# Kernel tuning notes

Hardware: AMD Instinct MI355X
Metric: run time of the kernel (lower is better)

The kernel has to match this reference:

```python
import math
import jax, jax.numpy as jnp
import numpy as np

B, T, T_P, C, H = 4, 2048, 256, 768, 12
HD = C // H


def setup_inputs() -> dict:
    key = jax.random.key(0)
    k1, k2, k3, k4 = jax.random.split(key, 4)
    x = jax.random.normal(k1, (B, T, C), dtype=jnp.float32)
    prefix = jax.random.normal(k2, (B, T_P, C), dtype=jnp.float32)
    # torch nn.Linear weight layout: (out_features, in_features)
    W_qkv = jax.random.normal(k3, (3 * C, C), dtype=jnp.float32) * (1.0 / math.sqrt(C))
    W_out = jax.random.normal(k4, (C, C), dtype=jnp.float32) * (1.0 / math.sqrt(C))
    return {"x": x, "prefix": prefix, "W_qkv": W_qkv, "W_out": W_out}


def _mac_causal_mask(t_p: int, t: int) -> jnp.ndarray:
    total = t_p + t
    mask = jnp.zeros((total, total), dtype=bool)
    mask = mask.at[:t_p, t_p:].set(True)  # h tokens blocked from x tokens
    causal = jnp.triu(jnp.ones((t, t), dtype=bool), k=1)  # causal within x block
    return mask.at[t_p:, t_p:].set(causal)


def reference(x, prefix, W_qkv, W_out):
    b, t, c = x.shape
    t_p = prefix.shape[1]
    t_all = t_p + t
    x_full = jnp.concatenate([prefix, x], axis=1)          # (B, T_all, C)
    qkv = x_full @ W_qkv.T                                  # (B, T_all, 3C)
    q, k, v = jnp.split(qkv, 3, axis=-1)
    # (B, H, T_all, HD)
    q = q.reshape(b, t_all, H, HD).transpose(0, 2, 1, 3)
    k = k.reshape(b, t_all, H, HD).transpose(0, 2, 1, 3)
    v = v.reshape(b, t_all, H, HD).transpose(0, 2, 1, 3)
    scale = 1.0 / math.sqrt(HD)
    att = jnp.einsum('bhqd,bhkd->bhqk', q, k) * scale       # (B, H, T_all, T_all)
    mask = _mac_causal_mask(t_p, t)
    att = jnp.where(mask[None, None], -jnp.inf, att)
    att = jax.nn.softmax(att, axis=-1)                      # dropout = identity (eval)
    out = jnp.einsum('bhqk,bhkd->bhqd', att, v)             # (B, H, T_all, HD)
    out = out.transpose(0, 2, 1, 3).reshape(b, t_all, c)
    out = out @ W_out.T
    return out[:, t_p:, :]                                  # only x portion (B, T, C)
```

## Files before the change

kernel.cpp:

```cpp
#include <hip/hip_runtime.h>

constexpr int Bn   = 4;
constexpr int Tn   = 2048;
constexpr int TPn  = 256;
constexpr int TALLn = 2304;
constexpr int Cn   = 768;
constexpr int Hn   = 12;
constexpr int HDn  = 64;

typedef __bf16 bf16x4 __attribute__((ext_vector_type(4)));
typedef __bf16 bf16x8 __attribute__((ext_vector_type(8)));
typedef float  f32x4  __attribute__((ext_vector_type(4)));
typedef unsigned u32x4 __attribute__((ext_vector_type(4)));

__device__ __forceinline__ unsigned short f2bf(float f) {
    unsigned int x = __float_as_uint(f);
    x += 0x7fffu + ((x >> 16) & 1u);
    return (unsigned short)(x >> 16);
}

__device__ __forceinline__ unsigned cvt_pk_bf16(float a, float b) {
    unsigned r;
    asm("v_cvt_pk_bf16_f32 %0, %1, %2" : "=v"(r) : "v"(a), "v"(b));
    return r;
}

#define ASYNC16(gsrc, ldst)                                                           \
    __builtin_amdgcn_global_load_lds((__attribute__((address_space(1))) void*)(gsrc), \
                                     (__attribute__((address_space(3))) void*)(ldst), \
                                     16, 0, 0)

__global__ __launch_bounds__(256) void k_prep(
        const float* __restrict__ x, const float* __restrict__ pre,
        const float* __restrict__ wqkv, const float* __restrict__ wout,
        unsigned short* __restrict__ xf, unsigned short* __restrict__ wqb,
        unsigned short* __restrict__ wob) {
    const int idx = blockIdx.x * 256 + threadIdx.x;
    constexpr int NXF = Bn * TALLn * Cn / 4;
    constexpr int NW1 = 3 * Cn * Cn / 4;
    const float* src;
    unsigned short* dst;
    if (idx < NXF) {
        const int row = idx / (Cn / 4);
        const int c   = (idx - row * (Cn / 4)) * 4;
        const int b = row / TALLn, tt = row - b * TALLn;
        src = (tt < TPn) ? pre + ((size_t)b * TPn + tt) * Cn + c
                         : x   + ((size_t)b * Tn + (tt - TPn)) * Cn + c;
        dst = xf + (size_t)row * Cn + c;
    } else {
        const int k = idx - NXF;
        if (k < NW1) { src = wqkv + (size_t)k * 4; dst = wqb + (size_t)k * 4; }
        else { src = wout + (size_t)(k - NW1) * 4; dst = wob + (size_t)(k - NW1) * 4; }
    }
    float4 f = *reinterpret_cast<const float4*>(src);
    ushort4 o = { f2bf(f.x), f2bf(f.y), f2bf(f.z), f2bf(f.w) };
    *reinterpret_cast<ushort4*>(dst) = o;
}

__global__ __launch_bounds__(256) void k_qkv_gemm(
        const unsigned short* __restrict__ A, const unsigned short* __restrict__ W,
        unsigned short* __restrict__ Qb, unsigned short* __restrict__ Kb,
        unsigned short* __restrict__ Vt) {
    __shared__ __align__(16) unsigned short smem[16384];
    const int tid  = threadIdx.x;
    const int wave = tid >> 6;
    const int lane = tid & 63;
    const int g = lane >> 4, l16 = lane & 15;
    const int m0 = blockIdx.x * 128, n0 = blockIdx.y * 128;
    const int wr = wave >> 1, wc = wave & 1;

    const unsigned short* pa[2];
    const unsigned short* pb[2];
    int sd[2];
    #pragma unroll
    for (int inst = 0; inst < 2; ++inst) {
        const int li = inst * 256 + tid;
        const int row = li >> 2;
        const int ch = (li & 3) ^ ((row >> 1) & 3);
        pa[inst] = A + (size_t)(m0 + row) * Cn + ch * 8;
        pb[inst] = W + (size_t)(n0 + row) * Cn + ch * 8;
        sd[inst] = (inst * 256 + wave * 64) * 8;
    }
    int aoff[4], boff[4];
    #pragma unroll
    for (int mt = 0; mt < 4; ++mt) {
        const int ra = wr * 64 + mt * 16 + l16;
        aoff[mt] = ra * 32 + ((g ^ ((ra >> 1) & 3)) << 3);
        const int rb = wc * 64 + mt * 16 + l16;
        boff[mt] = rb * 32 + ((g ^ ((rb >> 1) & 3)) << 3);
    }

    f32x4 acc[4][4] = {};

    #pragma unroll
    for (int inst = 0; inst < 2; ++inst) {
        ASYNC16(pa[inst], &smem[0]    + sd[inst]);
        ASYNC16(pb[inst], &smem[8192] + sd[inst]);
        pa[inst] += 32;
        pb[inst] += 32;
    }
    __syncthreads();

    int buf = 0;
    for (int kk = 0; kk < 24; ++kk) {
        if (kk + 1 < 24) {
            #pragma unroll
            for (int inst = 0; inst < 2; ++inst) {
                ASYNC16(pa[inst], &smem[(buf ^ 1) * 4096]        + sd[inst]);
                ASYNC16(pb[inst], &smem[8192 + (buf ^ 1) * 4096] + sd[inst]);
                pa[inst] += 32;
                pb[inst] += 32;
            }
        }
        const unsigned short* Ab = &smem[buf * 4096];
        const unsigned short* Bb = &smem[8192 + buf * 4096];
        bf16x8 af[4], bfv[4];
        #pragma unroll
        for (int mt = 0; mt < 4; ++mt) {
            af[mt]  = *reinterpret_cast<const bf16x8*>(&Ab[aoff[mt]]);
            bfv[mt] = *reinterpret_cast<const bf16x8*>(&Bb[boff[mt]]);
        }
        __builtin_amdgcn_s_setprio(1);
        #pragma unroll
        for (int mt = 0; mt < 4; ++mt)
            #pragma unroll
            for (int nt = 0; nt < 4; ++nt)
                acc[mt][nt] = __builtin_amdgcn_mfma_f32_16x16x32_bf16(
                        af[mt], bfv[nt], acc[mt][nt], 0, 0, 0);
        __builtin_amdgcn_s_setprio(0);
        buf ^= 1;
        __syncthreads();
    }

    const int b   = m0 / TALLn;
    const int t0  = m0 - b * TALLn;
    const int sel = n0 / Cn;
    const int hn0 = n0 - sel * Cn;
    constexpr float SCQ = 0.18033688011112042f;

    if (sel == 2) {
        #pragma unroll
        for (int mt = 0; mt < 4; ++mt)
            #pragma unroll
            for (int nt = 0; nt < 4; ++nt)
                #pragma unroll
                for (int r = 0; r < 4; ++r) {
                    const int t  = wr * 64 + mt * 16 + g * 4 + r;
                    const int hn = wc * 64 + nt * 16 + l16;
                    smem[hn * 128 + (((t >> 3) ^ (hn & 7)) << 3) + (t & 7)] =
                            f2bf(acc[mt][nt][r]);
                }
        __syncthreads();
        #pragma unroll
        for (int j = 0; j < 8; ++j) {
            const int u  = tid + 256 * j;
            const int hn = u >> 4, tc = u & 15;
            const int tile64 = tc >> 3;
            const int np = tc & 7;
            const int kg = np >> 2, gs = np & 3;
            const int tgA = tile64 * 8 + kg * 4 + (gs >> 1);
            const int sub = (gs & 1) * 4;
            bf16x4 rA = *reinterpret_cast<const bf16x4*>(
                    &smem[hn * 128 + ((tgA ^ (hn & 7)) << 3) + sub]);
            bf16x4 rB = *reinterpret_cast<const bf16x4*>(
                    &smem[hn * 128 + (((tgA + 2) ^ (hn & 7)) << 3) + sub]);
            bf16x8 v = __builtin_shufflevector(rA, rB, 0, 1, 2, 3, 4, 5, 6, 7);
            const int hh = (hn0 + hn) >> 6;
            const int dd = hn & 63;
            *reinterpret_cast<bf16x8*>(
                    &Vt[(((size_t)b * Hn + hh) * HDn + dd) * TALLn + t0 + tc * 8]) = v;
        }
    } else {
        #pragma unroll
        for (int mt = 0; mt < 4; ++mt)
            #pragma unroll
            for (int nt = 0; nt < 4; ++nt)
                #pragma unroll
                for (int r = 0; r < 4; ++r) {
                    const int t  = t0 + wr * 64 + mt * 16 + g * 4 + r;
                    const int hn = hn0 + wc * 64 + nt * 16 + l16;
                    const int h = hn >> 6, d = hn & 63;
                    if (sel == 0)
                        Qb[(((size_t)b * Hn + h) * TALLn + t) * HDn + d] =
                                f2bf(acc[mt][nt][r] * SCQ);
                    else
                        Kb[(((size_t)b * Hn + h) * TALLn + t) * HDn + d] =
                                f2bf(acc[mt][nt][r]);
                }
    }
}

__global__ __launch_bounds__(128) void k_attn(
        const unsigned short* __restrict__ Qb, const unsigned short* __restrict__ Kb,
        const unsigned short* __restrict__ Vt, unsigned short* __restrict__ Ob) {
    __shared__ __align__(16) unsigned short Ks[2][4096];
    __shared__ __align__(16) unsigned short Vs[2][4096];
    const int tid  = threadIdx.x;
    const int wave = tid >> 6;
    const int lane = tid & 63;
    const int l16  = lane & 15;
    const int g    = lane >> 4;

    const int fb  = blockIdx.x;
    const int j   = fb >> 3;
    const int bh  = 6 * (fb & 7) + (j % 6);
    const int chunk = 31 - (j / 6);
    const int nkt = 5 + chunk;
    const size_t kv = (size_t)bh * TALLn * HDn;

    int koff[4][2];
    #pragma unroll
    for (int band = 0; band < 4; ++band)
        #pragma unroll
        for (int ks = 0; ks < 2; ++ks)
            koff[band][ks] = (band * 16 + l16) * 64 + (((ks * 4 + g) ^ (l16 & 7)) << 3);
    int voff[2];
    #pragma unroll
    for (int kg = 0; kg < 2; ++kg)
        voff[kg] = l16 * 64 + (((kg * 4 + g) ^ (l16 & 7)) << 3);
    const unsigned short* pk[4];
    const unsigned short* pv[4];
    int sdst[4];
    #pragma unroll
    for (int inst = 0; inst < 4; ++inst) {
        const int li = inst * 128 + tid;
        const int row = li >> 3;
        const int ch = (li & 7) ^ (row & 7);
        pk[inst] = Kb + kv + row * HDn + ch * 8;
        pv[inst] = Vt + kv + row * TALLn + ch * 8;
        sdst[inst] = (inst * 128 + wave * 64) * 8;
    }
    constexpr int KSTRIDE = 64 * HDn;
    constexpr int VSTRIDE = 64;

    bf16x8 qfA[2], qfB[2];
    {
        const int tq = TPn + chunk * 64 + wave * 32 + l16;
        #pragma unroll
        for (int ks = 0; ks < 2; ++ks) {
            qfA[ks] = *reinterpret_cast<const bf16x8*>(
                    Qb + kv + (size_t)tq * HDn + ks * 32 + g * 8);
            qfB[ks] = *reinterpret_cast<const bf16x8*>(
                    Qb + kv + (size_t)(tq + 16) * HDn + ks * 32 + g * 8);
        }
    }

    bf16x8 ones;
    #pragma unroll
    for (int i = 0; i < 8; ++i) ones[i] = (__bf16)1.0f;

    f32x4 oaccA[4] = {}, oaccB[4] = {};
    f32x4 laccA = {}, laccB = {};

    #pragma unroll
    for (int inst = 0; inst < 4; ++inst) {
        ASYNC16(pk[inst], &Ks[0][0] + sdst[inst]);
        ASYNC16(pv[inst], &Vs[0][0] + sdst[inst]);
        pk[inst] += KSTRIDE;
        pv[inst] += VSTRIDE;
    }
    __syncthreads();

    int buf = 0;
    for (int t = 0; t < nkt; ++t) {
        if (t + 1 < nkt) {
            #pragma unroll
            for (int inst = 0; inst < 4; ++inst) {
                ASYNC16(pk[inst], &Ks[buf ^ 1][0] + sdst[inst]);
                ASYNC16(pv[inst], &Vs[buf ^ 1][0] + sdst[inst]);
                pk[inst] += KSTRIDE;
                pv[inst] += VSTRIDE;
            }
        }
        const unsigned short* Ksb = &Ks[buf][0];
        const unsigned short* Vsb = &Vs[buf][0];

        f32x4 sA[4] = {}, sB[4] = {};
        __builtin_amdgcn_s_setprio(1);
        #pragma unroll
        for (int band = 0; band < 4; ++band) {
            bf16x8 k0 = *reinterpret_cast<const bf16x8*>(&Ksb[koff[band][0]]);
            bf16x8 k1 = *reinterpret_cast<const bf16x8*>(&Ksb[koff[band][1]]);
            sA[band] = __builtin_amdgcn_mfma_f32_16x16x32_bf16(k0, qfA[0], sA[band], 0, 0, 0);
            sA[band] = __builtin_amdgcn_mfma_f32_16x16x32_bf16(k1, qfA[1], sA[band], 0, 0, 0);
            sB[band] = __builtin_amdgcn_mfma_f32_16x16x32_bf16(k0, qfB[0], sB[band], 0, 0, 0);
            sB[band] = __builtin_amdgcn_mfma_f32_16x16x32_bf16(k1, qfB[1], sB[band], 0, 0, 0);
        }
        __builtin_amdgcn_s_setprio(0);

        if (t == nkt - 1) {
            const int limA = wave * 32 + l16;
            #pragma unroll
            for (int band = 0; band < 4; ++band)
                #pragma unroll
                for (int r = 0; r < 4; ++r) {
                    const int key = band * 16 + g * 4 + r;
                    sA[band][r] = (key <= limA)      ? sA[band][r] : -1e30f;
                    sB[band][r] = (key <= limA + 16) ? sB[band][r] : -1e30f;
                }
        }

        unsigned dwA[4][2], dwB[4][2];
        #pragma unroll
        for (int band = 0; band < 4; ++band) {
            dwA[band][0] = cvt_pk_bf16(exp2f(sA[band][0]), exp2f(sA[band][1]));
            dwA[band][1] = cvt_pk_bf16(exp2f(sA[band][2]), exp2f(sA[band][3]));
            dwB[band][0] = cvt_pk_bf16(exp2f(sB[band][0]), exp2f(sB[band][1]));
            dwB[band][1] = cvt_pk_bf16(exp2f(sB[band][2]), exp2f(sB[band][3]));
        }

        __builtin_amdgcn_s_setprio(1);
        #pragma unroll
        for (int kg = 0; kg < 2; ++kg) {
            const u32x4 uA = { dwA[2 * kg][0], dwA[2 * kg][1],
                               dwA[2 * kg + 1][0], dwA[2 * kg + 1][1] };
            const u32x4 uB = { dwB[2 * kg][0], dwB[2 * kg][1],
                               dwB[2 * kg + 1][0], dwB[2 * kg + 1][1] };
            const bf16x8 pfA = __builtin_bit_cast(bf16x8, uA);
            const bf16x8 pfB = __builtin_bit_cast(bf16x8, uB);
            laccA = __builtin_amdgcn_mfma_f32_16x16x32_bf16(ones, pfA, laccA, 0, 0, 0);
            laccB = __builtin_amdgcn_mfma_f32_16x16x32_bf16(ones, pfB, laccB, 0, 0, 0);
            #pragma unroll
            for (int dband = 0; dband < 4; ++dband) {
                bf16x8 vf = *reinterpret_cast<const bf16x8*>(
                        &Vsb[dband * 1024 + voff[kg]]);
                oaccA[dband] = __builtin_amdgcn_mfma_f32_16x16x32_bf16(
                        vf, pfA, oaccA[dband], 0, 0, 0);
                oaccB[dband] = __builtin_amdgcn_mfma_f32_16x16x32_bf16(
                        vf, pfB, oaccB[dband], 0, 0, 0);
            }
        }
        __builtin_amdgcn_s_setprio(0);

        buf ^= 1;
        __syncthreads();
    }

    const int b = bh / Hn, h = bh - b * Hn;
    const float invA = 1.0f / laccA[0];
    const float invB = 1.0f / laccB[0];
    const size_t rowA = (size_t)b * Tn + chunk * 64 + wave * 32 + l16;
    #pragma unroll
    for (int dband = 0; dband < 4; ++dband) {
        ushort4 st;
        st.x = f2bf(oaccA[dband][0] * invA);
        st.y = f2bf(oaccA[dband][1] * invA);
        st.z = f2bf(oaccA[dband][2] * invA);
        st.w = f2bf(oaccA[dband][3] * invA);
        *reinterpret_cast<ushort4*>(&Ob[rowA * Cn + h * 64 + dband * 16 + g * 4]) = st;
        st.x = f2bf(oaccB[dband][0] * invB);
        st.y = f2bf(oaccB[dband][1] * invB);
        st.z = f2bf(oaccB[dband][2] * invB);
        st.w = f2bf(oaccB[dband][3] * invB);
        *reinterpret_cast<ushort4*>(&Ob[(rowA + 16) * Cn + h * 64 + dband * 16 + g * 4]) = st;
    }
}

__global__ __launch_bounds__(256) void k_out_gemm(
        const unsigned short* __restrict__ A, const unsigned short* __restrict__ W,
        float* __restrict__ out) {
    __shared__ __align__(16) unsigned short smem[16384];
    const int tid  = threadIdx.x;
    const int wave = tid >> 6;
    const int lane = tid & 63;
    const int g = lane >> 4, l16 = lane & 15;
    const int m0 = blockIdx.x * 128, n0 = blockIdx.y * 128;
    const int wr = wave >> 1, wc = wave & 1;

    const unsigned short* pa[2];
    const unsigned short* pb[2];
    int sd[2];
    #pragma unroll
    for (int inst = 0; inst < 2; ++inst) {
        const int li = inst * 256 + tid;
        const int row = li >> 2;
        const int ch = (li & 3) ^ ((row >> 1) & 3);
        pa[inst] = A + (size_t)(m0 + row) * Cn + ch * 8;
        pb[inst] = W + (size_t)(n0 + row) * Cn + ch * 8;
        sd[inst] = (inst * 256 + wave * 64) * 8;
    }
    int aoff[4], boff[4];
    #pragma unroll
    for (int mt = 0; mt < 4; ++mt) {
        const int ra = wr * 64 + mt * 16 + l16;
        aoff[mt] = ra * 32 + ((g ^ ((ra >> 1) & 3)) << 3);
        const int rb = wc * 64 + mt * 16 + l16;
        boff[mt] = rb * 32 + ((g ^ ((rb >> 1) & 3)) << 3);
    }

    f32x4 acc[4][4] = {};

    #pragma unroll
    for (int inst = 0; inst < 2; ++inst) {
        ASYNC16(pa[inst], &smem[0]    + sd[inst]);
        ASYNC16(pb[inst], &smem[8192] + sd[inst]);
        pa[inst] += 32;
        pb[inst] += 32;
    }
    __syncthreads();

    int buf = 0;
    for (int kk = 0; kk < 24; ++kk) {
        if (kk + 1 < 24) {
            #pragma unroll
            for (int inst = 0; inst < 2; ++inst) {
                ASYNC16(pa[inst], &smem[(buf ^ 1) * 4096]        + sd[inst]);
                ASYNC16(pb[inst], &smem[8192 + (buf ^ 1) * 4096] + sd[inst]);
                pa[inst] += 32;
                pb[inst] += 32;
            }
        }
        const unsigned short* Ab = &smem[buf * 4096];
        const unsigned short* Bb = &smem[8192 + buf * 4096];
        bf16x8 af[4], bfv[4];
        #pragma unroll
        for (int mt = 0; mt < 4; ++mt) {
            af[mt]  = *reinterpret_cast<const bf16x8*>(&Ab[aoff[mt]]);
            bfv[mt] = *reinterpret_cast<const bf16x8*>(&Bb[boff[mt]]);
        }
        __builtin_amdgcn_s_setprio(1);
        #pragma unroll
        for (int mt = 0; mt < 4; ++mt)
            #pragma unroll
            for (int nt = 0; nt < 4; ++nt)
                acc[mt][nt] = __builtin_amdgcn_mfma_f32_16x16x32_bf16(
                        af[mt], bfv[nt], acc[mt][nt], 0, 0, 0);
        __builtin_amdgcn_s_setprio(0);
        buf ^= 1;
        __syncthreads();
    }

    #pragma unroll
    for (int mt = 0; mt < 4; ++mt)
        #pragma unroll
        for (int nt = 0; nt < 4; ++nt)
            #pragma unroll
            for (int r = 0; r < 4; ++r) {
                const int m = m0 + wr * 64 + mt * 16 + g * 4 + r;
                const int n = n0 + wc * 64 + nt * 16 + l16;
                out[(size_t)m * Cn + n] = acc[mt][nt][r];
            }
}

extern "C" void kernel_launch(void* const* d_in, const int* in_sizes, int n_in,
                              void* d_out, int out_size, void* d_ws, size_t ws_size,
                              hipStream_t stream) {
    const float* x    = (const float*)d_in[0];
    const float* pre  = (const float*)d_in[1];
    const float* wqkv = (const float*)d_in[2];
    const float* wout = (const float*)d_in[3];
    float* out = (float*)d_out;
    char* ws = (char*)d_ws;

    unsigned short* xf  = (unsigned short*)(ws + 0);
    unsigned short* wqb = (unsigned short*)(ws + 14155776);
    unsigned short* wob = (unsigned short*)(ws + 17694720);
    unsigned short* Qb  = (unsigned short*)(ws + 18874368);
    unsigned short* Kb  = (unsigned short*)(ws + 33030144);
    unsigned short* Vt  = (unsigned short*)(ws + 47185920);
    unsigned short* Ob  = (unsigned short*)(ws + 61341696);

    constexpr int PREP_UNITS = (Bn * TALLn * Cn + 4 * Cn * Cn) / 4;
    k_prep<<<dim3(PREP_UNITS / 256), 256, 0, stream>>>(x, pre, wqkv, wout, xf, wqb, wob);
    k_qkv_gemm<<<dim3((Bn * TALLn) / 128, (3 * Cn) / 128), 256, 0, stream>>>(
            xf, wqb, Qb, Kb, Vt);
    k_attn<<<dim3(1536), 128, 0, stream>>>(Qb, Kb, Vt, Ob);
    k_out_gemm<<<dim3((Bn * Tn) / 128, Cn / 128), 256, 0, stream>>>(Ob, wob, out);
}
```

Baseline: 158.6 us.

## Split attention key range across two wave pairs and merge partials in LDS

Doubles the attention block to four waves, with two wave pairs each processing half of the key tiles for the same query rows in separate double-buffered LDS regions. Partial output accumulators and row sums from the second pair are written to reused LDS and added by the first pair before normalization and store. This shortens the serial key loop per block for long causal rows, at the cost of more LDS per block, a cross-wave reduction, and possible loss of occupancy.

```diff
diff --git a/kernel.cpp b/kernel.cpp
--- a/kernel.cpp
+++ b/kernel.cpp
@@ -190,13 +190,15 @@
     }
 }
 
-__global__ __launch_bounds__(128) void k_attn(
+__global__ __launch_bounds__(256) void k_attn(
         const unsigned short* __restrict__ Qb, const unsigned short* __restrict__ Kb,
         const unsigned short* __restrict__ Vt, unsigned short* __restrict__ Ob) {
-    __shared__ __align__(16) unsigned short Ks[2][4096];
-    __shared__ __align__(16) unsigned short Vs[2][4096];
+    __shared__ __align__(16) unsigned short Ks[2][2][4096];
+    __shared__ __align__(16) unsigned short Vs[2][2][4096];
     const int tid  = threadIdx.x;
     const int wave = tid >> 6;
+    const int pair = wave >> 1;
+    const int qh   = wave & 1;
     const int lane = tid & 63;
     const int l16  = lane & 15;
     const int g    = lane >> 4;
@@ -206,6 +208,9 @@
     const int bh  = 6 * (fb & 7) + (j % 6);
     const int chunk = 31 - (j / 6);
     const int nkt = 5 + chunk;
+    const int na  = nkt >> 1;
+    const int myN = pair ? (nkt - na) : na;
+    const int nit = nkt - na;
     const size_t kv = (size_t)bh * TALLn * HDn;
 
     int koff[4][2];
@@ -218,24 +223,33 @@
     #pragma unroll
     for (int kg = 0; kg < 2; ++kg)
         voff[kg] = l16 * 64 + (((kg * 4 + g) ^ (l16 & 7)) << 3);
+
     const unsigned short* pk[4];
     const unsigned short* pv[4];
     int sdst[4];
+    const int keybase = pair ? na * 64 : 0;
     #pragma unroll
     for (int inst = 0; inst < 4; ++inst) {
-        const int li = inst * 128 + tid;
-        const int row = li >> 3;
-        const int ch = (li & 7) ^ (row & 7);
-        pk[inst] = Kb + kv + row * HDn + ch * 8;
-        pv[inst] = Vt + kv + row * TALLn + ch * 8;
-        sdst[inst] = (inst * 128 + wave * 64) * 8;
-    }
-    constexpr int KSTRIDE = 64 * HDn;
-    constexpr int VSTRIDE = 64;
+        const int gi = inst * 128 + (tid & 127);
+        const int row = gi >> 3;
+        const int ch = (gi & 7) ^ (row & 7);
+        pk[inst] = Kb + kv + (size_t)(keybase + row) * HDn + ch * 8;
+        pv[inst] = Vt + kv + (size_t)row * TALLn + keybase + ch * 8;
+        sdst[inst] = (inst * 128 + qh * 64) * 8;
+    }
+    auto stageKV = [&](int bs) {
+        #pragma unroll
+        for (int inst = 0; inst < 4; ++inst) {
+            ASYNC16(pk[inst], &Ks[pair][bs][0] + sdst[inst]);
+            ASYNC16(pv[inst], &Vs[pair][bs][0] + sdst[inst]);
+            pk[inst] += 64 * HDn;
+            pv[inst] += 64;
+        }
+    };
 
     bf16x8 qfA[2], qfB[2];
     {
-        const int tq = TPn + chunk * 64 + wave * 32 + l16;
+        const int tq = TPn + chunk * 64 + qh * 32 + l16;
         #pragma unroll
         for (int ks = 0; ks < 2; ++ks) {
             qfA[ks] = *reinterpret_cast<const bf16x8*>(
@@ -252,107 +266,119 @@
     f32x4 oaccA[4] = {}, oaccB[4] = {};
     f32x4 laccA = {}, laccB = {};
 
-    #pragma unroll
-    for (int inst = 0; inst < 4; ++inst) {
-        ASYNC16(pk[inst], &Ks[0][0] + sdst[inst]);
-        ASYNC16(pv[inst], &Vs[0][0] + sdst[inst]);
-        pk[inst] += KSTRIDE;
-        pv[inst] += VSTRIDE;
-    }
+    stageKV(0);
     __syncthreads();
 
     int buf = 0;
-    for (int t = 0; t < nkt; ++t) {
-        if (t + 1 < nkt) {
-            #pragma unroll
-            for (int inst = 0; inst < 4; ++inst) {
-                ASYNC16(pk[inst], &Ks[buf ^ 1][0] + sdst[inst]);
-                ASYNC16(pv[inst], &Vs[buf ^ 1][0] + sdst[inst]);
-                pk[inst] += KSTRIDE;
-                pv[inst] += VSTRIDE;
-            }
-        }
-        const unsigned short* Ksb = &Ks[buf][0];
-        const unsigned short* Vsb = &Vs[buf][0];
-
-        f32x4 sA[4] = {}, sB[4] = {};
-        __builtin_amdgcn_s_setprio(1);
-        #pragma unroll
-        for (int band = 0; band < 4; ++band) {
-            bf16x8 k0 = *reinterpret_cast<const bf16x8*>(&Ksb[koff[band][0]]);
-            bf16x8 k1 = *reinterpret_cast<const bf16x8*>(&Ksb[koff[band][1]]);
-            sA[band] = __builtin_amdgcn_mfma_f32_16x16x32_bf16(k0, qfA[0], sA[band], 0, 0, 0);
-            sA[band] = __builtin_amdgcn_mfma_f32_16x16x32_bf16(k1, qfA[1], sA[band], 0, 0, 0);
-            sB[band] = __builtin_amdgcn_mfma_f32_16x16x32_bf16(k0, qfB[0], sB[band], 0, 0, 0);
-            sB[band] = __builtin_amdgcn_mfma_f32_16x16x32_bf16(k1, qfB[1], sB[band], 0, 0, 0);
-        }
-        __builtin_amdgcn_s_setprio(0);
-
-        if (t == nkt - 1) {
-            const int limA = wave * 32 + l16;
-            #pragma unroll
-            for (int band = 0; band < 4; ++band)
+    for (int t = 0; t < nit; ++t) {
+        if (t < myN) {
+            if (t + 1 < myN) stageKV(buf ^ 1);
+            const unsigned short* Ksb = &Ks[pair][buf][0];
+            const unsigned short* Vsb = &Vs[pair][buf][0];
+
+            f32x4 sA[4] = {}, sB[4] = {};
+            __builtin_amdgcn_s_setprio(1);
+            #pragma unroll
+            for (int band = 0; band < 4; ++band) {
+                bf16x8 k0 = *reinterpret_cast<const bf16x8*>(&Ksb[koff[band][0]]);
+                bf16x8 k1 = *reinterpret_cast<const bf16x8*>(&Ksb[koff[band][1]]);
+                sA[band] = __builtin_amdgcn_mfma_f32_16x16x32_bf16(k0, qfA[0], sA[band], 0, 0, 0);
+                sA[band] = __builtin_amdgcn_mfma_f32_16x16x32_bf16(k1, qfA[1], sA[band], 0, 0, 0);
+                sB[band] = __builtin_amdgcn_mfma_f32_16x16x32_bf16(k0, qfB[0], sB[band], 0, 0, 0);
+                sB[band] = __builtin_amdgcn_mfma_f32_16x16x32_bf16(k1, qfB[1], sB[band], 0, 0, 0);
+            }
+            __builtin_amdgcn_s_setprio(0);
+
+            if (pair == 1 && t == myN - 1) {
+                const int limA = qh * 32 + l16;
                 #pragma unroll
-                for (int r = 0; r < 4; ++r) {
-                    const int key = band * 16 + g * 4 + r;
-                    sA[band][r] = (key <= limA)      ? sA[band][r] : -1e30f;
-                    sB[band][r] = (key <= limA + 16) ? sB[band][r] : -1e30f;
+                for (int band = 0; band < 4; ++band)
+                    #pragma unroll
+                    for (int r = 0; r < 4; ++r) {
+                        const int key = band * 16 + g * 4 + r;
+                        sA[band][r] = (key <= limA)      ? sA[band][r] : -1e30f;
+                        sB[band][r] = (key <= limA + 16) ? sB[band][r] : -1e30f;
+                    }
+            }
+
+            unsigned dwA[4][2], dwB[4][2];
+            #pragma unroll
+            for (int band = 0; band < 4; ++band) {
+                dwA[band][0] = cvt_pk_bf16(exp2f(sA[band][0]), exp2f(sA[band][1]));
+                dwA[band][1] = cvt_pk_bf16(exp2f(sA[band][2]), exp2f(sA[band][3]));
+                dwB[band][0] = cvt_pk_bf16(exp2f(sB[band][0]), exp2f(sB[band][1]));
+                dwB[band][1] = cvt_pk_bf16(exp2f(sB[band][2]), exp2f(sB[band][3]));
+            }
+
+            __builtin_amdgcn_s_setprio(1);
+            #pragma unroll
+            for (int kg = 0; kg < 2; ++kg) {
+                const u32x4 uA = { dwA[2 * kg][0], dwA[2 * kg][1],
+                                   dwA[2 * kg + 1][0], dwA[2 * kg + 1][1] };
+                const u32x4 uB = { dwB[2 * kg][0], dwB[2 * kg][1],
+                                   dwB[2 * kg + 1][0], dwB[2 * kg + 1][1] };
+                const bf16x8 pfA = __builtin_bit_cast(bf16x8, uA);
+                const bf16x8 pfB = __builtin_bit_cast(bf16x8, uB);
+                laccA = __builtin_amdgcn_mfma_f32_16x16x32_bf16(ones, pfA, laccA, 0, 0, 0);
+                laccB = __builtin_amdgcn_mfma_f32_16x16x32_bf16(ones, pfB, laccB, 0, 0, 0);
+                #pragma unroll
+                for (int dband = 0; dband < 4; ++dband) {
+                    bf16x8 vf = *reinterpret_cast<const bf16x8*>(
+                            &Vsb[dband * 1024 + voff[kg]]);
+                    oaccA[dband] = __builtin_amdgcn_mfma_f32_16x16x32_bf16(
+                            vf, pfA, oaccA[dband], 0, 0, 0);
+                    oaccB[dband] = __builtin_amdgcn_mfma_f32_16x16x32_bf16(
+                            vf, pfB, oaccB[dband], 0, 0, 0);
                 }
-        }
-
-        unsigned dwA[4][2], dwB[4][2];
-        #pragma unroll
-        for (int band = 0; band < 4; ++band) {
-            dwA[band][0] = cvt_pk_bf16(exp2f(sA[band][0]), exp2f(sA[band][1]));
-            dwA[band][1] = cvt_pk_bf16(exp2f(sA[band][2]), exp2f(sA[band][3]));
-            dwB[band][0] = cvt_pk_bf16(exp2f(sB[band][0]), exp2f(sB[band][1]));
-            dwB[band][1] = cvt_pk_bf16(exp2f(sB[band][2]), exp2f(sB[band][3]));
-        }
-
-        __builtin_amdgcn_s_setprio(1);
-        #pragma unroll
-        for (int kg = 0; kg < 2; ++kg) {
-            const u32x4 uA = { dwA[2 * kg][0], dwA[2 * kg][1],
-                               dwA[2 * kg + 1][0], dwA[2 * kg + 1][1] };
-            const u32x4 uB = { dwB[2 * kg][0], dwB[2 * kg][1],
-                               dwB[2 * kg + 1][0], dwB[2 * kg + 1][1] };
-            const bf16x8 pfA = __builtin_bit_cast(bf16x8, uA);
-            const bf16x8 pfB = __builtin_bit_cast(bf16x8, uB);
-            laccA = __builtin_amdgcn_mfma_f32_16x16x32_bf16(ones, pfA, laccA, 0, 0, 0);
-            laccB = __builtin_amdgcn_mfma_f32_16x16x32_bf16(ones, pfB, laccB, 0, 0, 0);
-            #pragma unroll
-            for (int dband = 0; dband < 4; ++dband) {
-                bf16x8 vf = *reinterpret_cast<const bf16x8*>(
-                        &Vsb[dband * 1024 + voff[kg]]);
-                oaccA[dband] = __builtin_amdgcn_mfma_f32_16x16x32_bf16(
-                        vf, pfA, oaccA[dband], 0, 0, 0);
-                oaccB[dband] = __builtin_amdgcn_mfma_f32_16x16x32_bf16(
-                        vf, pfB, oaccB[dband], 0, 0, 0);
-            }
-        }
-        __builtin_amdgcn_s_setprio(0);
-
-        buf ^= 1;
+            }
+            __builtin_amdgcn_s_setprio(0);
+            buf ^= 1;
+        }
         __syncthreads();
     }
 
-    const int b = bh / Hn, h = bh - b * Hn;
-    const float invA = 1.0f / laccA[0];
-    const float invB = 1.0f / laccB[0];
-    const size_t rowA = (size_t)b * Tn + chunk * 64 + wave * 32 + l16;
-    #pragma unroll
-    for (int dband = 0; dband < 4; ++dband) {
-        ushort4 st;
-        st.x = f2bf(oaccA[dband][0] * invA);
-        st.y = f2bf(oaccA[dband][1] * invA);
-        st.z = f2bf(oaccA[dband][2] * invA);
-        st.w = f2bf(oaccA[dband][3] * invA);
-        *reinterpret_cast<ushort4*>(&Ob[rowA * Cn + h * 64 + dband * 16 + g * 4]) = st;
-        st.x = f2bf(oaccB[dband][0] * invB);
-        st.y = f2bf(oaccB[dband][1] * invB);
-        st.z = f2bf(oaccB[dband][2] * invB);
-        st.w = f2bf(oaccB[dband][3] * invB);
-        *reinterpret_cast<ushort4*>(&Ob[(rowA + 16) * Cn + h * 64 + dband * 16 + g * 4]) = st;
+    float* fo = reinterpret_cast<float*>(&Ks[0][0][0]);
+    float* fl = reinterpret_cast<float*>(&Vs[0][0][0]);
+    if (pair == 1) {
+        #pragma unroll
+        for (int dband = 0; dband < 4; ++dband) {
+            *reinterpret_cast<f32x4*>(
+                    &fo[(((qh * 2 + 0) * 4 + dband) * 64 + lane) * 4]) = oaccA[dband];
+            *reinterpret_cast<f32x4*>(
+                    &fo[(((qh * 2 + 1) * 4 + dband) * 64 + lane) * 4]) = oaccB[dband];
+        }
+        fl[(qh * 2 + 0) * 64 + lane] = laccA[0];
+        fl[(qh * 2 + 1) * 64 + lane] = laccB[0];
+    }
+    __syncthreads();
+    if (pair == 0) {
+        #pragma unroll
+        for (int dband = 0; dband < 4; ++dband) {
+            oaccA[dband] += *reinterpret_cast<const f32x4*>(
+                    &fo[(((qh * 2 + 0) * 4 + dband) * 64 + lane) * 4]);
+            oaccB[dband] += *reinterpret_cast<const f32x4*>(
+                    &fo[(((qh * 2 + 1) * 4 + dband) * 64 + lane) * 4]);
+        }
+        const float invA = 1.0f / (laccA[0] + fl[(qh * 2 + 0) * 64 + lane]);
+        const float invB = 1.0f / (laccB[0] + fl[(qh * 2 + 1) * 64 + lane]);
+        const int b = bh / Hn, h = bh - b * Hn;
+        const size_t rowA = (size_t)b * Tn + chunk * 64 + qh * 32 + l16;
+        #pragma unroll
+        for (int dband = 0; dband < 4; ++dband) {
+            ushort4 st;
+            st.x = f2bf(oaccA[dband][0] * invA);
+            st.y = f2bf(oaccA[dband][1] * invA);
+            st.z = f2bf(oaccA[dband][2] * invA);
+            st.w = f2bf(oaccA[dband][3] * invA);
+            *reinterpret_cast<ushort4*>(
+                    &Ob[rowA * Cn + h * 64 + dband * 16 + g * 4]) = st;
+            st.x = f2bf(oaccB[dband][0] * invB);
+            st.y = f2bf(oaccB[dband][1] * invB);
+            st.z = f2bf(oaccB[dband][2] * invB);
+            st.w = f2bf(oaccB[dband][3] * invB);
+            *reinterpret_cast<ushort4*>(
+                    &Ob[(rowA + 16) * Cn + h * 64 + dband * 16 + g * 4]) = st;
+        }
     }
 }
 
@@ -464,6 +490,6 @@
     k_prep<<<dim3(PREP_UNITS / 256), 256, 0, stream>>>(x, pre, wqkv, wout, xf, wqb, wob);
     k_qkv_gemm<<<dim3((Bn * TALLn) / 128, (3 * Cn) / 128), 256, 0, stream>>>(
             xf, wqb, Qb, Kb, Vt);
-    k_attn<<<dim3(1536), 128, 0, stream>>>(Qb, Kb, Vt, Ob);
+    k_attn<<<dim3(1536), 256, 0, stream>>>(Qb, Kb, Vt, Ob);
     k_out_gemm<<<dim3((Bn * Tn) / 128, Cn / 128), 256, 0, stream>>>(Ob, wob, out);
 }
```

After: 148.4 us. -6.4%, faster.
